# Performance work log

Measured on AMD Instinct MI355X. Metric: run time of the kernel, lower is better.

Reference implementation:

```python
import jax, jax.numpy as jnp
import numpy as np

H = 128          # hidden_size
B = 64           # batch of users
T = 20           # current-session length (== max_sess_len)
S = 10           # friend sessions per user (graph degree)
L = 20           # max_sess_len
NUM_ITEMS = 50000
NUM_USERS = 10000
TOPK = 2         # topk in sess_similarity


def gru(x, W_ih, W_hh, b_ih, b_hh):
    """torch nn.GRU (1 layer, batch_first). x: [N, T, H] -> outputs [N, T, H], h_T [N, H]."""
    h0 = jnp.zeros((x.shape[0], x.shape[-1]), x.dtype)

    def step(h, xt):
        gi = xt @ W_ih.T + b_ih          # [N, 3H]
        gh = h @ W_hh.T + b_hh
        i_r, i_z, i_n = jnp.split(gi, 3, axis=-1)
        h_r, h_z, h_n = jnp.split(gh, 3, axis=-1)
        r = jax.nn.sigmoid(i_r + h_r)
        z = jax.nn.sigmoid(i_z + h_z)
        n = jnp.tanh(i_n + r * h_n)
        h = (1.0 - z) * n + z * h
        return h, h

    hT, ys = jax.lax.scan(step, h0, jnp.swapaxes(x, 0, 1))
    return jnp.swapaxes(ys, 0, 1), hT


def masked_softmax(x, mask, axis):
    neg = jnp.finfo(x.dtype).min
    return jax.nn.softmax(jnp.where(mask, x, neg), axis=axis)


def setup_inputs() -> dict:
    key = jax.random.key(0)
    ks = jax.random.split(key, 12)
    users = jax.random.randint(ks[0], (B,), 0, NUM_USERS)
    cur_sess = jax.random.randint(ks[1], (B, T), 0, NUM_ITEMS)          # all valid -> full length
    hist_sess = jax.random.randint(ks[2], (B, S, L), 0, NUM_ITEMS)
    frds_sess = jax.random.randint(ks[3], (B, S, L), 0, NUM_ITEMS)
    cur_sess_len = jnp.full((B,), T, dtype=jnp.int32)
    # parameters
    v_emb = jax.random.uniform(ks[4], (NUM_ITEMS + 1, H), minval=-1.0, maxval=1.0)
    v_emb = v_emb.at[NUM_ITEMS].set(0.0)                                 # padding_idx row
    u_emb = jax.random.normal(ks[5], (NUM_USERS, H)) * (1.0 / np.sqrt(H))
    sc = 1.0 / np.sqrt(H)
    W_ih = jax.random.normal(ks[6], (3 * H, H)) * sc
    W_hh = jax.random.normal(ks[7], (3 * H, H)) * sc
    b_ih = jnp.zeros((3 * H,), jnp.float32)
    b_hh = jnp.zeros((3 * H,), jnp.float32)
    out1_w = jax.random.normal(ks[8], (NUM_ITEMS, 3 * H)) * (1.0 / np.sqrt(3 * H))
    out1_b = jnp.zeros((NUM_ITEMS,), jnp.float32)
    return dict(users=users, cur_sess=cur_sess, hist_sess=hist_sess, frds_sess=frds_sess,
                cur_sess_len=cur_sess_len, v_emb=v_emb, u_emb=u_emb,
                W_ih=W_ih, W_hh=W_hh, b_ih=b_ih, b_hh=b_hh, out1_w=out1_w, out1_b=out1_b)


def reference(users, cur_sess, hist_sess, frds_sess, cur_sess_len,
              v_emb, u_emb, W_ih, W_hh, b_ih, b_hh, out1_w, out1_b):
    # --- rnn_encoder on current session (dropout p=0, eval) ---
    hs, _ = gru(v_emb[cur_sess], W_ih, W_hh, b_ih, b_hh)                 # [B, T, H]
    query = hs

    # --- friend branch (hist branch is dead: hu is overwritten with zeros) ---
    # sess_encoder: GRU over each friend session's items
    frd_items = v_emb[frds_sess]                                         # [B, S, L, H]
    enc, _ = gru(frd_items.reshape(B * S, L, H), W_ih, W_hh, b_ih, b_hh)
    enc = enc.reshape(B, S, L, H)                                        # encoder_output

    # sess_similarity: max over session positions, softmax over degree (S)
    scores = jnp.einsum('bth,bslh->bstl', query, enc)                    # [B, S, T, L]
    sim_raw = scores.max(axis=-1)                                        # [B, S, T]
    sim1 = jax.nn.softmax(sim_raw, axis=1)
    # preserve: edges that are top-2 most similar for ANY step t (S > TOPK branch)
    _, idx = jax.lax.top_k(jnp.swapaxes(sim1, 1, 2), TOPK)               # [B, T, 2]
    preserve = jax.nn.one_hot(idx, S, dtype=jnp.float32).sum((1, 2)) > 0 # [B, S]

    # sess_embedding_attn on the filtered subgraph (masking == filtering here)
    user_e = u_emb[users]                                                # [B, H]
    w = jax.nn.softmax(jnp.einsum('bh,bslh->bsl', user_e, frd_items), axis=2)
    sess_emb = jnp.einsum('bsl,bslh->bsh', w, frd_items)                 # [B, S, H]

    # user_sess_reduce_func: sim1 (pre-filter softmax values), then two softmaxes
    # over the surviving edges (masked softmax over S)
    m = preserve[:, :, None]                                             # [B, S, 1]
    s = masked_softmax(sim1, m, axis=1)
    s = masked_softmax(s, m, axis=1)
    s = jnp.where(m, s, 0.0)
    hf = jnp.einsum('bst,bsh->bth', s, sess_emb)                         # [B, T, H]

    hu = jnp.zeros_like(hs)                                              # hu = zeros_like(hs)
    output = jnp.concatenate([hs, hu, hf], axis=-1)                      # [B, T, 3H]
    logits = output @ out1_w.T + out1_b                                  # [B, T, NUM_ITEMS]
    return logits
```

## Files before the change

kernel.cpp:

```cpp
#include <hip/hip_runtime.h>
#include <cstdint>
#include <cstddef>

#define H_      128
#define B_      64
#define T_      20
#define S_      10
#define L_      20
#define NITEMS  50000
#define NSEQ    704
#define NTOK    (NSEQ * 20)
#define NPAD    50048
#define KA      256

typedef __attribute__((ext_vector_type(8))) short short8;
typedef __attribute__((ext_vector_type(4))) float f32x4;

__device__ __forceinline__ unsigned short f2bf(float f) {
  unsigned int u = __float_as_uint(f);
  u += 0x7FFF + ((u >> 16) & 1);
  return (unsigned short)(u >> 16);
}
__device__ __forceinline__ float sigmoidf_(float x) {
  return 1.0f / (1.0f + __expf(-x));
}

__global__ void __launch_bounds__(384) k2_gi(const int* __restrict__ cur,
                                             const int* __restrict__ frd,
                                             const float* __restrict__ vemb,
                                             const float* __restrict__ Wih,
                                             const float* __restrict__ bih,
                                             float* __restrict__ gi) {
  __shared__ float xs[16 * 128];
  __shared__ int ids[16];
  int tid = threadIdx.x;
  int tok0 = blockIdx.x * 16;
  if (tid < 16) {
    int tok = tok0 + tid;
    int seq = tok / 20, tt = tok % 20;
    ids[tid] = (seq < 64) ? cur[seq * 20 + tt] : frd[(seq - 64) * 20 + tt];
  }
  __syncthreads();
  for (int idx = tid; idx < 512; idx += 384) {
    int i = idx >> 5, kc = idx & 31;
    *(float4*)&xs[i * 128 + kc * 4] =
        *(const float4*)&vemb[(size_t)ids[i] * 128 + kc * 4];
  }
  __syncthreads();
  int j  = tid % 192;
  int th = tid / 192;
  float acc0[8], acc1[8];
#pragma unroll
  for (int i = 0; i < 8; i++) { acc0[i] = 0.f; acc1[i] = 0.f; }
  const float* wr0 = Wih + (size_t)j * 128;
  const float* wr1 = Wih + (size_t)(j + 192) * 128;
  const float* xb = &xs[th * 8 * 128];
  for (int kc = 0; kc < 32; kc++) {
    float4 wa = *(const float4*)(wr0 + kc * 4);
    float4 wc = *(const float4*)(wr1 + kc * 4);
#pragma unroll
    for (int i = 0; i < 8; i++) {
      float4 x4 = *(const float4*)&xb[i * 128 + kc * 4];
      acc0[i] += wa.x * x4.x + wa.y * x4.y + wa.z * x4.z + wa.w * x4.w;
      acc1[i] += wc.x * x4.x + wc.y * x4.y + wc.z * x4.z + wc.w * x4.w;
    }
  }
  float ba = bih[j], bc = bih[j + 192];
#pragma unroll
  for (int i = 0; i < 8; i++) {
    size_t row = (size_t)(tok0 + th * 8 + i) * 384;
    gi[row + j]       = acc0[i] + ba;
    gi[row + j + 192] = acc1[i] + bc;
  }
}

__global__ void __launch_bounds__(384) k3_gru(const float* __restrict__ Whh,
                                              const float* __restrict__ bhh,
                                              const float* __restrict__ gi,
                                              float* __restrict__ out_h) {
  __shared__ float hb[3 * 128];
  __shared__ float pre[3 * 256];
  __shared__ float gin[3 * 128];
  __shared__ float ghn[3 * 128];
  int j = threadIdx.x;
  int seq0 = blockIdx.x * 3;
  int G = NSEQ - seq0; if (G > 3) G = 3;
  float4 wv[32];
  const float4* wr = (const float4*)(Whh + (size_t)j * 128);
#pragma unroll
  for (int kc = 0; kc < 32; kc++) wv[kc] = wr[kc];
  float bb = bhh[j];
  if (j < 128) { hb[j] = 0.f; hb[128 + j] = 0.f; hb[256 + j] = 0.f; }
  __syncthreads();
  for (int t = 0; t < 20; t++) {
    for (int g = 0; g < G; g++) {
      float acc = bb;
#pragma unroll
      for (int kc = 0; kc < 32; kc++) {
        float4 h4 = *(const float4*)&hb[g * 128 + kc * 4];
        float4 w4 = wv[kc];
        acc += w4.x * h4.x + w4.y * h4.y + w4.z * h4.z + w4.w * h4.w;
      }
      float gv = gi[(size_t)((seq0 + g) * 20 + t) * 384 + j];
      if (j < 256) pre[g * 256 + j] = gv + acc;
      else { gin[g * 128 + (j - 256)] = gv; ghn[g * 128 + (j - 256)] = acc; }
    }
    __syncthreads();
    if (j < 128) {
      for (int g = 0; g < G; g++) {
        float r = sigmoidf_(pre[g * 256 + j]);
        float z = sigmoidf_(pre[g * 256 + 128 + j]);
        float n = tanhf(gin[g * 128 + j] + r * ghn[g * 128 + j]);
        float hN = (1.f - z) * n + z * hb[g * 128 + j];
        hb[g * 128 + j] = hN;
        out_h[(size_t)((seq0 + g) * 20 + t) * 128 + j] = hN;
      }
    }
    __syncthreads();
  }
}

__global__ void __launch_bounds__(256) k4_scores(const float* __restrict__ out_h,
                                                 float* __restrict__ sim_raw) {
  __shared__ float qs[20 * 132];
  __shared__ float es[20 * 132];
  __shared__ float sc[400];
  int tid = threadIdx.x;
  int b = blockIdx.x / 10, s = blockIdx.x % 10;
  int eseq = 64 + b * 10 + s;
  for (int idx = tid; idx < 640; idx += 256) {
    int row = idx >> 5, kc = idx & 31;
    *(float4*)&qs[row * 132 + kc * 4] =
        *(const float4*)&out_h[(size_t)(b * 20 + row) * 128 + kc * 4];
    *(float4*)&es[row * 132 + kc * 4] =
        *(const float4*)&out_h[(size_t)(eseq * 20 + row) * 128 + kc * 4];
  }
  __syncthreads();
  for (int idx = tid; idx < 400; idx += 256) {
    int t = idx / 20, l = idx % 20;
    float acc = 0.f;
#pragma unroll
    for (int kc = 0; kc < 32; kc++) {
      float4 q4 = *(const float4*)&qs[t * 132 + kc * 4];
      float4 e4 = *(const float4*)&es[l * 132 + kc * 4];
      acc += q4.x * e4.x + q4.y * e4.y + q4.z * e4.z + q4.w * e4.w;
    }
    sc[idx] = acc;
  }
  __syncthreads();
  if (tid < 20) {
    float m = sc[tid * 20];
    for (int l = 1; l < 20; l++) m = fmaxf(m, sc[tid * 20 + l]);
    sim_raw[(size_t)(b * 10 + s) * 20 + tid] = m;
  }
}

__global__ void __launch_bounds__(128) k6_sess(const int* __restrict__ users,
                                               const int* __restrict__ frd,
                                               const float* __restrict__ vemb,
                                               const float* __restrict__ uemb,
                                               float* __restrict__ sess) {
  __shared__ float fs[20 * 132];
  __shared__ float us[128];
  __shared__ float dt[20];
  __shared__ float wl[20];
  __shared__ int fid[20];
  int tid = threadIdx.x;
  int b = blockIdx.x / 10, s = blockIdx.x % 10;
  if (tid < 20) fid[tid] = frd[(size_t)(b * 10 + s) * 20 + tid];
  us[tid] = uemb[(size_t)users[b] * 128 + tid];
  __syncthreads();
  for (int idx = tid; idx < 640; idx += 128) {
    int row = idx >> 5, kc = idx & 31;
    *(float4*)&fs[row * 132 + kc * 4] =
        *(const float4*)&vemb[(size_t)fid[row] * 128 + kc * 4];
  }
  __syncthreads();
  if (tid < 20) {
    float acc = 0.f;
    for (int kc = 0; kc < 32; kc++) {
      float4 u4 = *(const float4*)&us[kc * 4];
      float4 f4 = *(const float4*)&fs[tid * 132 + kc * 4];
      acc += u4.x * f4.x + u4.y * f4.y + u4.z * f4.z + u4.w * f4.w;
    }
    dt[tid] = acc;
  }
  __syncthreads();
  if (tid < 20) {
    float mx = -3.4e38f;
    for (int l = 0; l < 20; l++) mx = fmaxf(mx, dt[l]);
    float sum = 0.f;
    for (int l = 0; l < 20; l++) sum += __expf(dt[l] - mx);
    wl[tid] = __expf(dt[tid] - mx) / sum;
  }
  __syncthreads();
  float acc = 0.f;
  for (int l = 0; l < 20; l++) acc += wl[l] * fs[l * 132 + tid];
  sess[(size_t)(b * 10 + s) * 128 + tid] = acc;
}

__global__ void __launch_bounds__(256) k5_fused(const float* __restrict__ sim_raw,
                                                const float* __restrict__ sess,
                                                const float* __restrict__ out_h,
                                                unsigned int* __restrict__ act) {
  __shared__ float sv[200];
  __shared__ float s1[200];
  __shared__ float sf[200];
  __shared__ float se[10 * 128];
  __shared__ int pres[10];
  int tid = threadIdx.x;
  int b = blockIdx.x;
  for (int idx = tid; idx < 200; idx += 256) sv[idx] = sim_raw[(size_t)b * 200 + idx];
  for (int idx = tid; idx < 1280; idx += 256) se[idx] = sess[(size_t)b * 1280 + idx];
  if (tid < 10) pres[tid] = 0;
  __syncthreads();
  if (tid < 20) {
    int t = tid;
    float mx = -3.4e38f;
    for (int s = 0; s < 10; s++) mx = fmaxf(mx, sv[s * 20 + t]);
    float sum = 0.f;
    for (int s = 0; s < 10; s++) sum += __expf(sv[s * 20 + t] - mx);
    float inv = 1.0f / sum;
    float v1 = -1.f, v2 = -1.f; int i1 = 0, i2 = 0;
    for (int s = 0; s < 10; s++) {
      float v = __expf(sv[s * 20 + t] - mx) * inv;
      s1[s * 20 + t] = v;
      if (v > v1) { v2 = v1; i2 = i1; v1 = v; i1 = s; }
      else if (v > v2) { v2 = v; i2 = s; }
    }
    atomicOr(&pres[i1], 1);
    atomicOr(&pres[i2], 1);
  }
  __syncthreads();
  if (tid < 20) {
    int t = tid;
    float mx = -3.4e38f;
    for (int s = 0; s < 10; s++) if (pres[s]) mx = fmaxf(mx, s1[s * 20 + t]);
    float sum = 0.f;
    for (int s = 0; s < 10; s++) if (pres[s]) sum += __expf(s1[s * 20 + t] - mx);
    float inv = 1.f / sum;
    float mx2 = -3.4e38f;
    for (int s = 0; s < 10; s++)
      if (pres[s]) mx2 = fmaxf(mx2, __expf(s1[s * 20 + t] - mx) * inv);
    float sum2 = 0.f;
    for (int s = 0; s < 10; s++)
      if (pres[s]) sum2 += __expf(__expf(s1[s * 20 + t] - mx) * inv - mx2);
    float inv2 = 1.f / sum2;
    for (int s = 0; s < 10; s++) {
      float o = 0.f;
      if (pres[s]) o = __expf(__expf(s1[s * 20 + t] - mx) * inv - mx2) * inv2;
      sf[s * 20 + t] = o;
    }
  }
  __syncthreads();
  for (int idx = tid; idx < 2560; idx += 256) {
    int t = idx >> 7, p = idx & 127;
    int m = b * 20 + t;
    float a0, a1;
    if (p < 64) {
      a0 = out_h[(size_t)m * 128 + p * 2];
      a1 = out_h[(size_t)m * 128 + p * 2 + 1];
    } else {
      int h0 = (p - 64) * 2;
      float acc0 = 0.f, acc1 = 0.f;
#pragma unroll
      for (int s = 0; s < 10; s++) {
        float w = sf[s * 20 + t];
        acc0 += w * se[s * 128 + h0];
        acc1 += w * se[s * 128 + h0 + 1];
      }
      a0 = acc0; a1 = acc1;
    }
    act[(size_t)m * 128 + p] = (unsigned)f2bf(a0) | ((unsigned)f2bf(a1) << 16);
  }
}

__device__ __forceinline__ void async_cp16(const unsigned short* g, unsigned short* l) {
  __builtin_amdgcn_global_load_lds((__attribute__((address_space(1))) void*)g,
                                   (__attribute__((address_space(3))) void*)l,
                                   16, 0, 0);
}

__global__ void __launch_bounds__(256) k9_gemm(const unsigned short* __restrict__ act,
                                               const float* __restrict__ w1,
                                               const float* __restrict__ bias,
                                               float* __restrict__ out) {
  __shared__ __align__(16) unsigned short Bs[128 * 256];
  __shared__ __align__(16) unsigned short As[2][128 * 32];
  int tid = threadIdx.x;
  int w = tid >> 6, lane = tid & 63;
  int q = (lane >> 4) & 3, c = lane & 15;
  int wm = w >> 1, wn = w & 1;
  int nb0 = blockIdx.x * 128;

  {
    int lhi = lane >> 2, llo = lane & 3;
#pragma unroll
    for (int i = 0; i < 2; i++) {
      int rbase = w * 32 + i * 16;
      int r = rbase + lhi;
      int sw = (r ^ (r >> 2)) & 3;
      const unsigned short* src = act + ((size_t)r * 256 + ((llo ^ sw) << 3));
      async_cp16(src, &As[0][rbase * 32]);
    }
  }

  {
    int kc = tid & 31;
    int src = (kc < 16) ? kc * 8 : kc * 8 + 128;
#pragma unroll 4
    for (int i = 0; i < 16; i++) {
      int row = i * 8 + (tid >> 5);
      int n = nb0 + row;
      unsigned int o0, o1, o2, o3;
      if (n < NITEMS) {
        const float* p = w1 + (size_t)n * 384 + src;
        float4 f0 = *(const float4*)p;
        float4 f1 = *(const float4*)(p + 4);
        o0 = (unsigned)f2bf(f0.x) | ((unsigned)f2bf(f0.y) << 16);
        o1 = (unsigned)f2bf(f0.z) | ((unsigned)f2bf(f0.w) << 16);
        o2 = (unsigned)f2bf(f1.x) | ((unsigned)f2bf(f1.y) << 16);
        o3 = (unsigned)f2bf(f1.z) | ((unsigned)f2bf(f1.w) << 16);
      } else {
        o0 = o1 = o2 = o3 = 0u;
      }
      int slot = kc ^ (row & 31);
      *(uint4*)&Bs[row * 256 + slot * 8] = make_uint4(o0, o1, o2, o3);
    }
  }

  float bs[4]; int okn[4]; int ncol[4];
#pragma unroll
  for (int nt = 0; nt < 4; nt++) {
    int n = nb0 + wn * 64 + nt * 16 + c;
    ncol[nt] = n;
    okn[nt] = (n < NITEMS);
    bs[nt] = (n < NITEMS) ? bias[n] : 0.f;
  }

  __syncthreads();

  f32x4 acc[4][4];
  int buf = 0;
  int lhi = lane >> 2, llo = lane & 3;
  for (int s = 0; s < 80; s++) {
    int mcs = s >> 3, kfs = s & 7;
    if (s + 1 < 80) {
      int mcn = (s + 1) >> 3, kfn = (s + 1) & 7;
#pragma unroll
      for (int i = 0; i < 2; i++) {
        int rbase = w * 32 + i * 16;
        int r = rbase + lhi;
        int sw = (r ^ (r >> 2)) & 3;
        const unsigned short* src =
            act + ((size_t)(mcn * 128 + r) * 256 + kfn * 32 + ((llo ^ sw) << 3));
        async_cp16(src, &As[buf ^ 1][rbase * 32]);
      }
    }
    if (kfs == 0) {
#pragma unroll
      for (int mt = 0; mt < 4; mt++)
#pragma unroll
        for (int nt = 0; nt < 4; nt++) {
          f32x4 z = {0.f, 0.f, 0.f, 0.f};
          acc[mt][nt] = z;
        }
    }
    short8 bfr[4];
#pragma unroll
    for (int nt = 0; nt < 4; nt++) {
      int n_l = wn * 64 + nt * 16 + c;
      int slot = n_l * 32 + ((kfs * 4 + q) ^ (n_l & 31));
      bfr[nt] = *(const short8*)&Bs[slot * 8];
    }
#pragma unroll
    for (int mt = 0; mt < 4; mt++) {
      int row = wm * 64 + mt * 16 + c;
      int sw = (row ^ (row >> 2)) & 3;
      short8 af = *(const short8*)&As[buf][row * 32 + ((q ^ sw) << 3)];
#pragma unroll
      for (int nt = 0; nt < 4; nt++)
        acc[mt][nt] = __builtin_amdgcn_mfma_f32_16x16x32_bf16(af, bfr[nt], acc[mt][nt], 0, 0, 0);
    }
    if (kfs == 7) {
#pragma unroll
      for (int nt = 0; nt < 4; nt++) {
        if (okn[nt]) {
#pragma unroll
          for (int mt = 0; mt < 4; mt++) {
            int m = mcs * 128 + wm * 64 + mt * 16 + q * 4;
#pragma unroll
            for (int r = 0; r < 4; r++)
              out[(size_t)(m + r) * NITEMS + ncol[nt]] = acc[mt][nt][r] + bs[nt];
          }
        }
      }
    }
    __syncthreads();
    buf ^= 1;
  }
}

extern "C" void kernel_launch(void* const* d_in, const int* in_sizes, int n_in,
                              void* d_out, int out_size, void* d_ws, size_t ws_size,
                              hipStream_t stream) {
  const int*   users = (const int*)d_in[0];
  const int*   cur   = (const int*)d_in[1];
  const int*   frd   = (const int*)d_in[3];
  const float* vemb  = (const float*)d_in[5];
  const float* uemb  = (const float*)d_in[6];
  const float* Wih   = (const float*)d_in[7];
  const float* Whh   = (const float*)d_in[8];
  const float* bih   = (const float*)d_in[9];
  const float* bhh   = (const float*)d_in[10];
  const float* w1    = (const float*)d_in[11];
  const float* b1    = (const float*)d_in[12];
  float* out = (float*)d_out;

  char* ws = (char*)d_ws;
  size_t off = 0;
  auto alloc = [&](size_t bytes) -> void* {
    void* p = ws + off;
    off = (off + bytes + 255) & ~(size_t)255;
    return p;
  };
  unsigned int*   act  = (unsigned int*)alloc((size_t)1280 * 128 * 4);
  float*          gi   = (float*)alloc((size_t)NTOK * 384 * 4);
  float*          outh = (float*)alloc((size_t)NTOK * 128 * 4);
  float*          simr = (float*)alloc((size_t)12800 * 4);
  float*          sess = (float*)alloc((size_t)640 * 128 * 4);

  k2_gi<<<NTOK / 16, 384, 0, stream>>>(cur, frd, vemb, Wih, bih, gi);
  k3_gru<<<(NSEQ + 2) / 3, 384, 0, stream>>>(Whh, bhh, gi, outh);
  k4_scores<<<640, 256, 0, stream>>>(outh, simr);
  k6_sess<<<640, 128, 0, stream>>>(users, frd, vemb, uemb, sess);
  k5_fused<<<64, 256, 0, stream>>>(simr, sess, outh, (unsigned int*)act);
  k9_gemm<<<NPAD / 128, 256, 0, stream>>>((const unsigned short*)act, w1, b1, out);
}
```

Measured before the change: 535.1 us.

## Pre-convert output weights to bf16, fuse score/session kernels, restructure GEMM and GRU

Adds a separate kernel that converts the output projection weights to bf16 in workspace, skipping the unused zero hu segment. The GEMM then async-loads B tiles from that buffer, and its double-buffered async A pipeline is replaced with synchronous padded-LDS loads. The score and session-embedding kernels are merged into one launch, and the GRU step is unrolled over three sequences to share weight registers. The weight conversion is still redone on every call, so it adds a full extra pass over the weights plus a bf16 write-back, and the GEMM loses its A-operand overlap.

```diff
diff --git a/kernel.cpp b/kernel.cpp
--- a/kernel.cpp
+++ b/kernel.cpp
@@ -23,6 +23,27 @@
 }
 __device__ __forceinline__ float sigmoidf_(float x) {
   return 1.0f / (1.0f + __expf(-x));
+}
+
+__global__ void __launch_bounds__(256) k1_convert_w(const float* __restrict__ w,
+                                                    unsigned short* __restrict__ wb) {
+  int t = blockIdx.x * 256 + threadIdx.x;
+  int n = t >> 5, kc = t & 31;
+  int k0 = kc * 8;
+  unsigned int o0, o1, o2, o3;
+  if (n < NITEMS) {
+    int src = (k0 < 128) ? k0 : (k0 + 128);
+    const float* p = w + (size_t)n * 384 + src;
+    float4 f0 = *(const float4*)p;
+    float4 f1 = *(const float4*)(p + 4);
+    o0 = (unsigned)f2bf(f0.x) | ((unsigned)f2bf(f0.y) << 16);
+    o1 = (unsigned)f2bf(f0.z) | ((unsigned)f2bf(f0.w) << 16);
+    o2 = (unsigned)f2bf(f1.x) | ((unsigned)f2bf(f1.y) << 16);
+    o3 = (unsigned)f2bf(f1.z) | ((unsigned)f2bf(f1.w) << 16);
+  } else {
+    o0 = o1 = o2 = o3 = 0u;
+  }
+  *(uint4*)(wb + (size_t)n * 256 + k0) = make_uint4(o0, o1, o2, o3);
 }
 
 __global__ void __launch_bounds__(384) k2_gi(const int* __restrict__ cur,
@@ -92,90 +113,117 @@
   float bb = bhh[j];
   if (j < 128) { hb[j] = 0.f; hb[128 + j] = 0.f; hb[256 + j] = 0.f; }
   __syncthreads();
-  for (int t = 0; t < 20; t++) {
-    for (int g = 0; g < G; g++) {
-      float acc = bb;
+  if (G == 3) {
+    for (int t = 0; t < 20; t++) {
+      float a0 = bb, a1 = bb, a2 = bb;
 #pragma unroll
       for (int kc = 0; kc < 32; kc++) {
-        float4 h4 = *(const float4*)&hb[g * 128 + kc * 4];
         float4 w4 = wv[kc];
-        acc += w4.x * h4.x + w4.y * h4.y + w4.z * h4.z + w4.w * h4.w;
-      }
-      float gv = gi[(size_t)((seq0 + g) * 20 + t) * 384 + j];
-      if (j < 256) pre[g * 256 + j] = gv + acc;
-      else { gin[g * 128 + (j - 256)] = gv; ghn[g * 128 + (j - 256)] = acc; }
-    }
-    __syncthreads();
-    if (j < 128) {
+        float4 h0 = *(const float4*)&hb[0 * 128 + kc * 4];
+        float4 h1 = *(const float4*)&hb[1 * 128 + kc * 4];
+        float4 h2 = *(const float4*)&hb[2 * 128 + kc * 4];
+        a0 += w4.x * h0.x + w4.y * h0.y + w4.z * h0.z + w4.w * h0.w;
+        a1 += w4.x * h1.x + w4.y * h1.y + w4.z * h1.z + w4.w * h1.w;
+        a2 += w4.x * h2.x + w4.y * h2.y + w4.z * h2.z + w4.w * h2.w;
+      }
+      float g0 = gi[(size_t)((seq0 + 0) * 20 + t) * 384 + j];
+      float g1 = gi[(size_t)((seq0 + 1) * 20 + t) * 384 + j];
+      float g2 = gi[(size_t)((seq0 + 2) * 20 + t) * 384 + j];
+      if (j < 256) {
+        pre[0 * 256 + j] = g0 + a0;
+        pre[1 * 256 + j] = g1 + a1;
+        pre[2 * 256 + j] = g2 + a2;
+      } else {
+        gin[0 * 128 + (j - 256)] = g0; ghn[0 * 128 + (j - 256)] = a0;
+        gin[1 * 128 + (j - 256)] = g1; ghn[1 * 128 + (j - 256)] = a1;
+        gin[2 * 128 + (j - 256)] = g2; ghn[2 * 128 + (j - 256)] = a2;
+      }
+      __syncthreads();
+      if (j < 128) {
+#pragma unroll
+        for (int g = 0; g < 3; g++) {
+          float r = sigmoidf_(pre[g * 256 + j]);
+          float z = sigmoidf_(pre[g * 256 + 128 + j]);
+          float n = tanhf(gin[g * 128 + j] + r * ghn[g * 128 + j]);
+          float hN = (1.f - z) * n + z * hb[g * 128 + j];
+          hb[g * 128 + j] = hN;
+          out_h[(size_t)((seq0 + g) * 20 + t) * 128 + j] = hN;
+        }
+      }
+      __syncthreads();
+    }
+  } else {
+    for (int t = 0; t < 20; t++) {
       for (int g = 0; g < G; g++) {
-        float r = sigmoidf_(pre[g * 256 + j]);
-        float z = sigmoidf_(pre[g * 256 + 128 + j]);
-        float n = tanhf(gin[g * 128 + j] + r * ghn[g * 128 + j]);
-        float hN = (1.f - z) * n + z * hb[g * 128 + j];
-        hb[g * 128 + j] = hN;
-        out_h[(size_t)((seq0 + g) * 20 + t) * 128 + j] = hN;
-      }
-    }
-    __syncthreads();
-  }
-}
-
-__global__ void __launch_bounds__(256) k4_scores(const float* __restrict__ out_h,
-                                                 float* __restrict__ sim_raw) {
+        float acc = bb;
+#pragma unroll
+        for (int kc = 0; kc < 32; kc++) {
+          float4 h4 = *(const float4*)&hb[g * 128 + kc * 4];
+          float4 w4 = wv[kc];
+          acc += w4.x * h4.x + w4.y * h4.y + w4.z * h4.z + w4.w * h4.w;
+        }
+        float gv = gi[(size_t)((seq0 + g) * 20 + t) * 384 + j];
+        if (j < 256) pre[g * 256 + j] = gv + acc;
+        else { gin[g * 128 + (j - 256)] = gv; ghn[g * 128 + (j - 256)] = acc; }
+      }
+      __syncthreads();
+      if (j < 128) {
+        for (int g = 0; g < G; g++) {
+          float r = sigmoidf_(pre[g * 256 + j]);
+          float z = sigmoidf_(pre[g * 256 + 128 + j]);
+          float n = tanhf(gin[g * 128 + j] + r * ghn[g * 128 + j]);
+          float hN = (1.f - z) * n + z * hb[g * 128 + j];
+          hb[g * 128 + j] = hN;
+          out_h[(size_t)((seq0 + g) * 20 + t) * 128 + j] = hN;
+        }
+      }
+      __syncthreads();
+    }
+  }
+}
+
+__global__ void __launch_bounds__(256) k46(const int* __restrict__ users,
+                                           const int* __restrict__ frd,
+                                           const float* __restrict__ vemb,
+                                           const float* __restrict__ uemb,
+                                           const float* __restrict__ out_h,
+                                           float* __restrict__ sim_raw,
+                                           float* __restrict__ sess) {
   __shared__ float qs[20 * 132];
   __shared__ float es[20 * 132];
+  __shared__ float fs[20 * 132];
   __shared__ float sc[400];
-  int tid = threadIdx.x;
-  int b = blockIdx.x / 10, s = blockIdx.x % 10;
-  int eseq = 64 + b * 10 + s;
-  for (int idx = tid; idx < 640; idx += 256) {
-    int row = idx >> 5, kc = idx & 31;
-    *(float4*)&qs[row * 132 + kc * 4] =
-        *(const float4*)&out_h[(size_t)(b * 20 + row) * 128 + kc * 4];
-    *(float4*)&es[row * 132 + kc * 4] =
-        *(const float4*)&out_h[(size_t)(eseq * 20 + row) * 128 + kc * 4];
-  }
-  __syncthreads();
-  for (int idx = tid; idx < 400; idx += 256) {
-    int t = idx / 20, l = idx % 20;
-    float acc = 0.f;
-#pragma unroll
-    for (int kc = 0; kc < 32; kc++) {
-      float4 q4 = *(const float4*)&qs[t * 132 + kc * 4];
-      float4 e4 = *(const float4*)&es[l * 132 + kc * 4];
-      acc += q4.x * e4.x + q4.y * e4.y + q4.z * e4.z + q4.w * e4.w;
-    }
-    sc[idx] = acc;
-  }
-  __syncthreads();
-  if (tid < 20) {
-    float m = sc[tid * 20];
-    for (int l = 1; l < 20; l++) m = fmaxf(m, sc[tid * 20 + l]);
-    sim_raw[(size_t)(b * 10 + s) * 20 + tid] = m;
-  }
-}
-
-__global__ void __launch_bounds__(128) k6_sess(const int* __restrict__ users,
-                                               const int* __restrict__ frd,
-                                               const float* __restrict__ vemb,
-                                               const float* __restrict__ uemb,
-                                               float* __restrict__ sess) {
-  __shared__ float fs[20 * 132];
   __shared__ float us[128];
   __shared__ float dt[20];
   __shared__ float wl[20];
   __shared__ int fid[20];
   int tid = threadIdx.x;
   int b = blockIdx.x / 10, s = blockIdx.x % 10;
+  int eseq = 64 + b * 10 + s;
   if (tid < 20) fid[tid] = frd[(size_t)(b * 10 + s) * 20 + tid];
-  us[tid] = uemb[(size_t)users[b] * 128 + tid];
-  __syncthreads();
-  for (int idx = tid; idx < 640; idx += 128) {
+  if (tid < 128) us[tid] = uemb[(size_t)users[b] * 128 + tid];
+  __syncthreads();
+  for (int idx = tid; idx < 640; idx += 256) {
     int row = idx >> 5, kc = idx & 31;
     *(float4*)&fs[row * 132 + kc * 4] =
         *(const float4*)&vemb[(size_t)fid[row] * 128 + kc * 4];
-  }
-  __syncthreads();
+    *(float4*)&qs[row * 132 + kc * 4] =
+        *(const float4*)&out_h[(size_t)(b * 20 + row) * 128 + kc * 4];
+    *(float4*)&es[row * 132 + kc * 4] =
+        *(const float4*)&out_h[(size_t)(eseq * 20 + row) * 128 + kc * 4];
+  }
+  __syncthreads();
+  for (int idx = tid; idx < 400; idx += 256) {
+    int t = idx / 20, l = idx % 20;
+    float acc = 0.f;
+#pragma unroll
+    for (int kc = 0; kc < 32; kc++) {
+      float4 q4 = *(const float4*)&qs[t * 132 + kc * 4];
+      float4 e4 = *(const float4*)&es[l * 132 + kc * 4];
+      acc += q4.x * e4.x + q4.y * e4.y + q4.z * e4.z + q4.w * e4.w;
+    }
+    sc[idx] = acc;
+  }
   if (tid < 20) {
     float acc = 0.f;
     for (int kc = 0; kc < 32; kc++) {
@@ -187,6 +235,9 @@
   }
   __syncthreads();
   if (tid < 20) {
+    float m = sc[tid * 20];
+    for (int l = 1; l < 20; l++) m = fmaxf(m, sc[tid * 20 + l]);
+    sim_raw[(size_t)(b * 10 + s) * 20 + tid] = m;
     float mx = -3.4e38f;
     for (int l = 0; l < 20; l++) mx = fmaxf(mx, dt[l]);
     float sum = 0.f;
@@ -194,9 +245,11 @@
     wl[tid] = __expf(dt[tid] - mx) / sum;
   }
   __syncthreads();
-  float acc = 0.f;
-  for (int l = 0; l < 20; l++) acc += wl[l] * fs[l * 132 + tid];
-  sess[(size_t)(b * 10 + s) * 128 + tid] = acc;
+  if (tid < 128) {
+    float acc = 0.f;
+    for (int l = 0; l < 20; l++) acc += wl[l] * fs[l * 132 + tid];
+    sess[(size_t)(b * 10 + s) * 128 + tid] = acc;
+  }
 }
 
 __global__ void __launch_bounds__(256) k5_fused(const float* __restrict__ sim_raw,
@@ -282,51 +335,24 @@
 }
 
 __global__ void __launch_bounds__(256) k9_gemm(const unsigned short* __restrict__ act,
-                                               const float* __restrict__ w1,
+                                               const unsigned short* __restrict__ wb,
                                                const float* __restrict__ bias,
                                                float* __restrict__ out) {
   __shared__ __align__(16) unsigned short Bs[128 * 256];
-  __shared__ __align__(16) unsigned short As[2][128 * 32];
+  __shared__ __align__(16) unsigned short As[128 * 40];
   int tid = threadIdx.x;
   int w = tid >> 6, lane = tid & 63;
   int q = (lane >> 4) & 3, c = lane & 15;
   int wm = w >> 1, wn = w & 1;
   int nb0 = blockIdx.x * 128;
 
-  {
-    int lhi = lane >> 2, llo = lane & 3;
-#pragma unroll
-    for (int i = 0; i < 2; i++) {
-      int rbase = w * 32 + i * 16;
-      int r = rbase + lhi;
-      int sw = (r ^ (r >> 2)) & 3;
-      const unsigned short* src = act + ((size_t)r * 256 + ((llo ^ sw) << 3));
-      async_cp16(src, &As[0][rbase * 32]);
-    }
-  }
-
-  {
-    int kc = tid & 31;
-    int src = (kc < 16) ? kc * 8 : kc * 8 + 128;
-#pragma unroll 4
-    for (int i = 0; i < 16; i++) {
-      int row = i * 8 + (tid >> 5);
-      int n = nb0 + row;
-      unsigned int o0, o1, o2, o3;
-      if (n < NITEMS) {
-        const float* p = w1 + (size_t)n * 384 + src;
-        float4 f0 = *(const float4*)p;
-        float4 f1 = *(const float4*)(p + 4);
-        o0 = (unsigned)f2bf(f0.x) | ((unsigned)f2bf(f0.y) << 16);
-        o1 = (unsigned)f2bf(f0.z) | ((unsigned)f2bf(f0.w) << 16);
-        o2 = (unsigned)f2bf(f1.x) | ((unsigned)f2bf(f1.y) << 16);
-        o3 = (unsigned)f2bf(f1.z) | ((unsigned)f2bf(f1.w) << 16);
-      } else {
-        o0 = o1 = o2 = o3 = 0u;
-      }
-      int slot = kc ^ (row & 31);
-      *(uint4*)&Bs[row * 256 + slot * 8] = make_uint4(o0, o1, o2, o3);
-    }
+#pragma unroll
+  for (int i = 0; i < 16; i++) {
+    int n_l = i * 8 + w * 2 + (lane >> 5);
+    int p = lane & 31;
+    int kc = p ^ (n_l & 31);
+    async_cp16(wb + (size_t)(nb0 + n_l) * 256 + kc * 8,
+               &Bs[(i * 8 + w * 2) * 256]);
   }
 
   float bs[4]; int okn[4]; int ncol[4];
@@ -338,66 +364,56 @@
     bs[nt] = (n < NITEMS) ? bias[n] : 0.f;
   }
 
-  __syncthreads();
-
-  f32x4 acc[4][4];
-  int buf = 0;
-  int lhi = lane >> 2, llo = lane & 3;
-  for (int s = 0; s < 80; s++) {
-    int mcs = s >> 3, kfs = s & 7;
-    if (s + 1 < 80) {
-      int mcn = (s + 1) >> 3, kfn = (s + 1) & 7;
-#pragma unroll
-      for (int i = 0; i < 2; i++) {
-        int rbase = w * 32 + i * 16;
-        int r = rbase + lhi;
-        int sw = (r ^ (r >> 2)) & 3;
-        const unsigned short* src =
-            act + ((size_t)(mcn * 128 + r) * 256 + kfn * 32 + ((llo ^ sw) << 3));
-        async_cp16(src, &As[buf ^ 1][rbase * 32]);
-      }
-    }
-    if (kfs == 0) {
-#pragma unroll
-      for (int mt = 0; mt < 4; mt++)
-#pragma unroll
-        for (int nt = 0; nt < 4; nt++) {
-          f32x4 z = {0.f, 0.f, 0.f, 0.f};
-          acc[mt][nt] = z;
+  for (int mc = 0; mc < 10; mc++) {
+    f32x4 acc[4][4];
+#pragma unroll
+    for (int mt = 0; mt < 4; mt++)
+#pragma unroll
+      for (int nt = 0; nt < 4; nt++) {
+        f32x4 z = {0.f, 0.f, 0.f, 0.f};
+        acc[mt][nt] = z;
+      }
+    for (int kf = 0; kf < 8; kf++) {
+      __syncthreads();
+      {
+        int ch0 = tid * 2;
+#pragma unroll
+        for (int jj = 0; jj < 2; jj++) {
+          int ch = ch0 + jj;
+          int row = ch >> 2, kk = ch & 3;
+          short8 v = *(const short8*)&act[(size_t)(mc * 128 + row) * 256 + kf * 32 + kk * 8];
+          *(short8*)&As[row * 40 + kk * 8] = v;
         }
-    }
-    short8 bfr[4];
+      }
+      __syncthreads();
+      short8 bfr[4];
+#pragma unroll
+      for (int nt = 0; nt < 4; nt++) {
+        int n_l = wn * 64 + nt * 16 + c;
+        int slot = n_l * 32 + ((kf * 4 + q) ^ (n_l & 31));
+        bfr[nt] = *(const short8*)&Bs[slot * 8];
+      }
+#pragma unroll
+      for (int mt = 0; mt < 4; mt++) {
+        int row = wm * 64 + mt * 16 + c;
+        short8 af = *(const short8*)&As[row * 40 + q * 8];
+#pragma unroll
+        for (int nt = 0; nt < 4; nt++)
+          acc[mt][nt] = __builtin_amdgcn_mfma_f32_16x16x32_bf16(af, bfr[nt], acc[mt][nt], 0, 0, 0);
+      }
+    }
 #pragma unroll
     for (int nt = 0; nt < 4; nt++) {
-      int n_l = wn * 64 + nt * 16 + c;
-      int slot = n_l * 32 + ((kfs * 4 + q) ^ (n_l & 31));
-      bfr[nt] = *(const short8*)&Bs[slot * 8];
-    }
-#pragma unroll
-    for (int mt = 0; mt < 4; mt++) {
-      int row = wm * 64 + mt * 16 + c;
-      int sw = (row ^ (row >> 2)) & 3;
-      short8 af = *(const short8*)&As[buf][row * 32 + ((q ^ sw) << 3)];
-#pragma unroll
-      for (int nt = 0; nt < 4; nt++)
-        acc[mt][nt] = __builtin_amdgcn_mfma_f32_16x16x32_bf16(af, bfr[nt], acc[mt][nt], 0, 0, 0);
-    }
-    if (kfs == 7) {
-#pragma unroll
-      for (int nt = 0; nt < 4; nt++) {
-        if (okn[nt]) {
-#pragma unroll
-          for (int mt = 0; mt < 4; mt++) {
-            int m = mcs * 128 + wm * 64 + mt * 16 + q * 4;
-#pragma unroll
-            for (int r = 0; r < 4; r++)
-              out[(size_t)(m + r) * NITEMS + ncol[nt]] = acc[mt][nt][r] + bs[nt];
-          }
+      if (okn[nt]) {
+#pragma unroll
+        for (int mt = 0; mt < 4; mt++) {
+          int m = mc * 128 + wm * 64 + mt * 16 + q * 4;
+#pragma unroll
+          for (int r = 0; r < 4; r++)
+            out[(size_t)(m + r) * NITEMS + ncol[nt]] = acc[mt][nt][r] + bs[nt];
         }
       }
     }
-    __syncthreads();
-    buf ^= 1;
   }
 }
 
@@ -424,16 +440,17 @@
     off = (off + bytes + 255) & ~(size_t)255;
     return p;
   };
+  unsigned short* wb   = (unsigned short*)alloc((size_t)NPAD * 256 * 2);
   unsigned int*   act  = (unsigned int*)alloc((size_t)1280 * 128 * 4);
   float*          gi   = (float*)alloc((size_t)NTOK * 384 * 4);
   float*          outh = (float*)alloc((size_t)NTOK * 128 * 4);
   float*          simr = (float*)alloc((size_t)12800 * 4);
   float*          sess = (float*)alloc((size_t)640 * 128 * 4);
 
+  k1_convert_w<<<NPAD / 8, 256, 0, stream>>>(w1, wb);
   k2_gi<<<NTOK / 16, 384, 0, stream>>>(cur, frd, vemb, Wih, bih, gi);
   k3_gru<<<(NSEQ + 2) / 3, 384, 0, stream>>>(Whh, bhh, gi, outh);
-  k4_scores<<<640, 256, 0, stream>>>(outh, simr);
-  k6_sess<<<640, 128, 0, stream>>>(users, frd, vemb, uemb, sess);
+  k46<<<640, 256, 0, stream>>>(users, frd, vemb, uemb, outh, simr, sess);
   k5_fused<<<64, 256, 0, stream>>>(simr, sess, outh, (unsigned int*)act);
-  k9_gemm<<<NPAD / 128, 256, 0, stream>>>((const unsigned short*)act, w1, b1, out);
-}
+  k9_gemm<<<NPAD / 128, 256, 0, stream>>>((const unsigned short*)act, wb, b1, out);
+}
```

Result: no change. 531.5 us (-0.7%).
